# Kernel tuning notes

Hardware: AMD Instinct MI355X
Metric: run time of the kernel (lower is better)

Reference implementation:

```python
import jax, jax.numpy as jnp
import numpy as np

N_NODES = 20000
N_EDGES = 640000
IN_DIM = 128
HID_DIM = 256
N_CLASSES = 3
N_TYPES = 4
N_ASPECTS = 4096


def _type_aware_gcn(x, W_type, W_self, b, src, dst, etypes, n_nodes):
    # Per-node, per-type transforms: [N, T, H]
    xt = jnp.einsum('nd,tdh->nth', x, W_type)
    # Per-edge message: transform of source node under the edge's type. [E, H]
    msg = xt[src, etypes]
    # Degree-normalized scatter-sum into destination nodes.
    agg = jax.ops.segment_sum(msg, dst, num_segments=n_nodes)
    deg = jax.ops.segment_sum(jnp.ones((src.shape[0],), dtype=x.dtype), dst,
                              num_segments=n_nodes)
    agg = agg / jnp.clip(deg, 1.0)[:, None]
    # Self-loop transform + bias.
    return agg + x @ W_self + b


def setup_inputs() -> dict:
    key = jax.random.key(0)
    ks = jax.random.split(key, 12)
    features = jax.random.normal(ks[0], (N_NODES, IN_DIM), dtype=jnp.float32)
    edge_index = jax.random.randint(ks[1], (2, N_EDGES), 0, N_NODES)
    edge_types = jax.random.randint(ks[2], (N_EDGES,), 0, N_TYPES)
    aspect_indices = jax.random.randint(ks[3], (N_ASPECTS,), 0, N_NODES)
    s1 = 1.0 / np.sqrt(IN_DIM)
    s2 = 1.0 / np.sqrt(HID_DIM)
    W_type1 = jax.random.uniform(ks[4], (N_TYPES, IN_DIM, HID_DIM), minval=-s1, maxval=s1)
    W_self1 = jax.random.uniform(ks[5], (IN_DIM, HID_DIM), minval=-s1, maxval=s1)
    b1 = jnp.zeros((HID_DIM,), dtype=jnp.float32)
    W_type2 = jax.random.uniform(ks[6], (N_TYPES, HID_DIM, HID_DIM), minval=-s2, maxval=s2)
    W_self2 = jax.random.uniform(ks[7], (HID_DIM, HID_DIM), minval=-s2, maxval=s2)
    b2 = jnp.zeros((HID_DIM,), dtype=jnp.float32)
    W_cls = jax.random.uniform(ks[8], (HID_DIM, N_CLASSES), minval=-s2, maxval=s2)
    b_cls = jnp.zeros((N_CLASSES,), dtype=jnp.float32)
    return {
        'features': features,
        'W_type1': W_type1, 'W_self1': W_self1, 'b1': b1,
        'W_type2': W_type2, 'W_self2': W_self2, 'b2': b2,
        'W_cls': W_cls, 'b_cls': b_cls,
        'edge_index': edge_index,
        'edge_types': edge_types,
        'aspect_indices': aspect_indices,
    }


def reference(features, W_type1, W_self1, b1, W_type2, W_self2, b2,
              W_cls, b_cls, edge_index, edge_types, aspect_indices):
    n = features.shape[0]
    src, dst = edge_index[0], edge_index[1]
    h = _type_aware_gcn(features, W_type1, W_self1, b1, src, dst, edge_types, n)
    h = jax.nn.relu(h)
    # dropout: eval mode -> identity
    h = _type_aware_gcn(h, W_type2, W_self2, b2, src, dst, edge_types, n)
    aspect_embeddings = h[aspect_indices]            # [A, H]
    logits = aspect_embeddings @ W_cls + b_cls       # [A, C]
    return logits
```

## Files before the change

kernel.cpp:

```cpp
#include <hip/hip_runtime.h>

#define N_NODES   20000
#define N_EDGES   640000
#define IN_DIM    128
#define HID_DIM   256
#define N_TYPES   4
#define N_ASPECTS 4096
#define NT4       (N_NODES * N_TYPES)
#define NBUCK     157
#define BCAP      5120
#define CHUNK     2560

typedef __bf16 v8bf __attribute__((ext_vector_type(8)));
typedef float  f32x4 __attribute__((ext_vector_type(4)));
typedef float  v2f   __attribute__((ext_vector_type(2)));

static __device__ __forceinline__ float bf2f(unsigned short u) {
    return __builtin_bit_cast(float, ((unsigned int)u) << 16);
}
static __device__ __forceinline__ float bflo(unsigned int u) {
    return __builtin_bit_cast(float, u << 16);
}
static __device__ __forceinline__ float bfhi(unsigned int u) {
    return __builtin_bit_cast(float, u & 0xffff0000u);
}
static __device__ __forceinline__ unsigned short f2bf(float f) {
    unsigned int u = __builtin_bit_cast(unsigned int, f);
    u += 0x7fffu + ((u >> 16) & 1u);
    return (unsigned short)(u >> 16);
}

static __device__ __forceinline__ void gload16(const unsigned short* g, unsigned short* l) {
    __builtin_amdgcn_global_load_lds(
        (const __attribute__((address_space(1))) void*)g,
        (__attribute__((address_space(3))) void*)l,
        16, 0, 0);
}

static __device__ __forceinline__ int local_flag(const unsigned short* w, int* red) {
    int tid = threadIdx.x;
    int c = 0;
    for (int i = tid; i < 1024; i += 256) {
        unsigned hb = (w[i] >> 8) & 0x7f;
        c += (hb >= 0x39 && hb <= 0x3D) ? 1 : 0;
    }
#pragma unroll
    for (int off = 32; off >= 1; off >>= 1) c += __shfl_down(c, off);
    if ((tid & 63) == 0) red[tid >> 6] = c;
    __syncthreads();
    int tot = red[0] + red[1] + red[2] + red[3];
    __syncthreads();
    return (tot >= 768) ? 1 : 0;
}

__global__ __launch_bounds__(256) void prepA_kernel(
        const void* __restrict__ x,
        const void* __restrict__ Ws1, const void* __restrict__ Wt1,
        const void* __restrict__ Ws2, const void* __restrict__ Wt2,
        const int* __restrict__ ei, const int* __restrict__ et,
        unsigned short* __restrict__ xc,
        unsigned int* __restrict__ xc8,
        unsigned short* __restrict__ WT1,
        unsigned short* __restrict__ WT2,
        int* __restrict__ bucket_cursor,
        unsigned int* __restrict__ breg,
        int* __restrict__ flag) {
    __shared__ __align__(16) char smem[14336];
    int b = blockIdx.x, tid = threadIdx.x;
    if (b < 250) {
        unsigned int* ord = (unsigned int*)smem;
        int* hist  = (int*)(smem + 10240);
        int* start = hist + NBUCK;
        int* cur   = start + NBUCK;
        int* gbase = cur + NBUCK;
        int* sbuf  = gbase + NBUCK;
        int e0 = b * CHUNK;
        for (int i = tid; i < NBUCK; i += 256) hist[i] = 0;
        __syncthreads();
        unsigned int pk[10];
        int bk[10];
#pragma unroll
        for (int r = 0; r < 10; r++) {
            int e = e0 + r * 256 + tid;
            int s = __builtin_nontemporal_load(ei + e);
            int d = __builtin_nontemporal_load(ei + N_EDGES + e);
            int t = __builtin_nontemporal_load(et + e);
            pk[r] = (unsigned int)s | ((unsigned int)t << 15) | ((unsigned int)d << 17);
            bk[r] = d >> 7;
            atomicAdd(&hist[bk[r]], 1);
        }
        __syncthreads();
        int v = (tid < NBUCK) ? hist[tid] : 0;
        sbuf[tid] = v;
        __syncthreads();
        for (int o = 1; o < 256; o <<= 1) {
            int t = (tid >= o) ? sbuf[tid - o] : 0;
            __syncthreads();
            sbuf[tid] += t;
            __syncthreads();
        }
        if (tid < NBUCK) { start[tid] = sbuf[tid] - v; cur[tid] = sbuf[tid] - v; }
        __syncthreads();
#pragma unroll
        for (int r = 0; r < 10; r++) {
            int p = atomicAdd(&cur[bk[r]], 1);
            ord[p] = pk[r];
        }
        __syncthreads();
        for (int bb = tid; bb < NBUCK; bb += 256)
            if (hist[bb] > 0) gbase[bb] = atomicAdd(bucket_cursor + bb, hist[bb]);
        __syncthreads();
        for (int p = tid; p < CHUNK; p += 256) {
            unsigned int e = ord[p];
            int bb = (int)(e >> 24);
            int gp = gbase[bb] + (p - start[bb]);
            if (gp < BCAP)
                __builtin_nontemporal_store(e, breg + (size_t)bb * BCAP + gp);
        }
    } else if (b < 1500) {
        int bf = local_flag((const unsigned short*)Ws1, (int*)smem);
        int idx = (b - 250) * 256 + tid;
        float f[8];
        if (bf) {
            uint4 v = reinterpret_cast<const uint4*>(x)[idx];
            reinterpret_cast<uint4*>(xc)[idx] = v;
            f[0] = bflo(v.x); f[1] = bfhi(v.x);
            f[2] = bflo(v.y); f[3] = bfhi(v.y);
            f[4] = bflo(v.z); f[5] = bfhi(v.z);
            f[6] = bflo(v.w); f[7] = bfhi(v.w);
        } else {
            const float* xf = reinterpret_cast<const float*>(x) + (size_t)idx * 8;
            unsigned short r[8] __attribute__((aligned(16)));
#pragma unroll
            for (int j = 0; j < 8; j++) { f[j] = xf[j]; r[j] = f2bf(xf[j]); }
            reinterpret_cast<uint4*>(xc)[idx] = *reinterpret_cast<const uint4*>(r);
        }
        int lo = 0, hi = 0;
        lo = __builtin_amdgcn_cvt_pk_fp8_f32(f[0], f[1], lo, false);
        lo = __builtin_amdgcn_cvt_pk_fp8_f32(f[2], f[3], lo, true);
        hi = __builtin_amdgcn_cvt_pk_fp8_f32(f[4], f[5], hi, false);
        hi = __builtin_amdgcn_cvt_pk_fp8_f32(f[6], f[7], hi, true);
        xc8[idx * 2]     = (unsigned int)lo;
        xc8[idx * 2 + 1] = (unsigned int)hi;
    } else if (b < 2140) {
        int bf = local_flag((const unsigned short*)Ws1, (int*)smem);
        int idx = (b - 1500) * 256 + tid;
        int n = idx / 640, k = idx - n * 640;
        const void* p = (k < 128) ? Ws1 : Wt1;
        size_t src = (k < 128) ? ((size_t)k * 256 + n) : ((size_t)(k - 128) * 256 + n);
        WT1[idx] = bf ? ((const unsigned short*)p)[src] : f2bf(((const float*)p)[src]);
    } else if (b < 3420) {
        int bf = local_flag((const unsigned short*)Ws1, (int*)smem);
        int idx = (b - 2140) * 256 + tid;
        int n = idx / 1280, k = idx - n * 1280;
        const void* p = (k < 256) ? Ws2 : Wt2;
        size_t src = (k < 256) ? ((size_t)k * 256 + n) : ((size_t)(k - 256) * 256 + n);
        WT2[idx] = bf ? ((const unsigned short*)p)[src] : f2bf(((const float*)p)[src]);
    } else {
        int bf = local_flag((const unsigned short*)Ws1, (int*)smem);
        if (tid == 0) *flag = bf;
    }
}

__global__ __launch_bounds__(256) void bucketB_kernel(
        const unsigned int* __restrict__ breg,
        const int* __restrict__ bucket_cursor,
        unsigned short* __restrict__ perm,
        int* __restrict__ offsets4) {
    __shared__ int cnt[512], off[512];
    __shared__ int buf[256], pscan[256];
    int b = blockIdx.x, tid = threadIdx.x;
    int cv = (tid < NBUCK) ? bucket_cursor[tid] : 0;
    if (cv > BCAP) cv = BCAP;
    buf[tid] = cv;
    __syncthreads();
    for (int o = 1; o < 256; o <<= 1) {
        int t = (tid >= o) ? buf[tid - o] : 0;
        __syncthreads();
        buf[tid] += t;
        __syncthreads();
    }
    int obase = (b > 0) ? buf[b - 1] : 0;
    if (b == 0 && tid == 0) offsets4[NT4] = buf[255];
    int Eb = bucket_cursor[b];
    if (Eb > BCAP) Eb = BCAP;
    for (int i = tid; i < 512; i += 256) cnt[i] = 0;
    __syncthreads();
    const unsigned int* reg = breg + (size_t)b * BCAP;
    for (int i = tid; i < Eb; i += 256) {
        unsigned int e = reg[i];
        int seg = (((e >> 17) & 127) << 2) | ((e >> 15) & 3);
        atomicAdd(&cnt[seg], 1);
    }
    __syncthreads();
    int pv = cnt[2 * tid] + cnt[2 * tid + 1];
    pscan[tid] = pv;
    __syncthreads();
    for (int o = 1; o < 256; o <<= 1) {
        int t = (tid >= o) ? pscan[tid - o] : 0;
        __syncthreads();
        pscan[tid] += t;
        __syncthreads();
    }
    int pexcl = pscan[tid] - pv;
    off[2 * tid]     = pexcl;
    off[2 * tid + 1] = pexcl + cnt[2 * tid];
    __syncthreads();
    for (int i = tid; i < 512; i += 256) {
        int node = b * 128 + (i >> 2);
        if (node < N_NODES) offsets4[node * 4 + (i & 3)] = obase + off[i];
    }
    __syncthreads();
    for (int i = tid; i < Eb; i += 256) {
        unsigned int e = reg[i];
        int seg = (((e >> 17) & 127) << 2) | ((e >> 15) & 3);
        int p = atomicAdd(&off[seg], 1);
        perm[obase + p] = (unsigned short)(e & 0x7fff);
    }
}

template <int D>
__global__ __launch_bounds__(256) void agg8_kernel(
        const unsigned int* __restrict__ F8,
        const int* __restrict__ offs4,
        const unsigned short* __restrict__ perm,
        unsigned short* __restrict__ AG) {
    constexpr int G = D / 8;
    constexpr int NSUB = 64 / G;
    int wave = threadIdx.x >> 6, lane = threadIdx.x & 63;
    int sg = lane / G;
    int gl = lane - sg * G;
    for (int n = blockIdx.x * 4 + wave; n < N_NODES; n += gridDim.x * 4) {
        int o0 = offs4[n * 4];
        int o4 = offs4[n * 4 + 4];
        int deg = o4 - o0;
        float inv = 1.0f / (float)(deg > 1 ? deg : 1);
        int s0 = o0;
#pragma unroll
        for (int t = 0; t < 4; t++) {
            int s1 = offs4[n * 4 + t + 1];
            float a[8];
#pragma unroll
            for (int v = 0; v < 8; v++) a[v] = 0.f;
            int j = s0;
            while (j < s1) {
                int m = s1 - j;
                if (m > 64) m = 64;
                int pw = (int)perm[j + ((lane < m) ? lane : 0)];
                int nfull = (m / (NSUB * 4)) * (NSUB * 4);
                for (int base = 0; base < nfull; base += NSUB * 4) {
                    uint2 x[4];
#pragma unroll
                    for (int l = 0; l < 4; l++) {
                        int src = __shfl(pw, base + sg * 4 + l);
                        x[l] = *reinterpret_cast<const uint2*>(F8 + (size_t)src * (D / 4) + gl * 2);
                    }
#pragma unroll
                    for (int l = 0; l < 4; l++) {
                        v2f p0 = __builtin_amdgcn_cvt_pk_f32_fp8((int)x[l].x, false);
                        v2f p1 = __builtin_amdgcn_cvt_pk_f32_fp8((int)x[l].x, true);
                        v2f p2 = __builtin_amdgcn_cvt_pk_f32_fp8((int)x[l].y, false);
                        v2f p3 = __builtin_amdgcn_cvt_pk_f32_fp8((int)x[l].y, true);
                        a[0] += p0.x; a[1] += p0.y;
                        a[2] += p1.x; a[3] += p1.y;
                        a[4] += p2.x; a[5] += p2.y;
                        a[6] += p3.x; a[7] += p3.y;
                    }
                }
                for (int k = nfull; k < m; k += NSUB) {
                    int e = k + sg;
                    int valid = (e < m);
                    int idx = valid ? e : (m - 1);
                    int src = __shfl(pw, idx);
                    uint2 x = *reinterpret_cast<const uint2*>(F8 + (size_t)src * (D / 4) + gl * 2);
                    unsigned msk = valid ? 0xffffffffu : 0u;
                    x.x &= msk; x.y &= msk;
                    v2f p0 = __builtin_amdgcn_cvt_pk_f32_fp8((int)x.x, false);
                    v2f p1 = __builtin_amdgcn_cvt_pk_f32_fp8((int)x.x, true);
                    v2f p2 = __builtin_amdgcn_cvt_pk_f32_fp8((int)x.y, false);
                    v2f p3 = __builtin_amdgcn_cvt_pk_f32_fp8((int)x.y, true);
                    a[0] += p0.x; a[1] += p0.y;
                    a[2] += p1.x; a[3] += p1.y;
                    a[4] += p2.x; a[5] += p2.y;
                    a[6] += p3.x; a[7] += p3.y;
                }
                j += m;
            }
#pragma unroll
            for (int v = 0; v < 8; v++) {
                float s = a[v];
                s += __shfl_xor(s, G);
                if (NSUB == 4) s += __shfl_xor(s, 2 * G);
                a[v] = s * inv;
            }
            if (sg == 0) {
                unsigned short r[8] __attribute__((aligned(16)));
#pragma unroll
                for (int v = 0; v < 8; v++) r[v] = f2bf(a[v]);
                *reinterpret_cast<uint4*>(AG + (size_t)n * (4 * D) + t * D + gl * 8) =
                    *reinterpret_cast<const uint4*>(r);
            }
            s0 = s1;
        }
    }
}

template <int D>
__global__ __launch_bounds__(256) void gemm_kernel(
        const unsigned short* __restrict__ X,
        const unsigned short* __restrict__ AG,
        const unsigned short* __restrict__ BT,
        const void* __restrict__ bias,
        const int* __restrict__ flagp,
        unsigned short* __restrict__ C,
        unsigned char* __restrict__ C8,
        int M, int relu) {
    constexpr int K = 5 * D;
    __shared__ __align__(16) unsigned short As[128 * 64];
    __shared__ __align__(16) unsigned short Bs[128 * 64];
    int b = blockIdx.x;
    int mt = (b >> 4) * 8 + (b & 7);
    int nt = (b >> 3) & 1;
    int mtiles = (M + 127) >> 7;
    if (mt >= mtiles) return;
    int m0 = mt * 128;
    int n0 = nt * 128;
    int tid  = threadIdx.x;
    int wave = tid >> 6, lane = tid & 63;
    int wm = wave >> 1, wn = wave & 1;
    int quad = lane >> 4, l16 = lane & 15;

    f32x4 acc[4][4];
#pragma unroll
    for (int i = 0; i < 4; i++)
#pragma unroll
        for (int j = 0; j < 4; j++) acc[i][j] = (f32x4){0.f, 0.f, 0.f, 0.f};

    for (int k0 = 0; k0 < K; k0 += 64) {
        const unsigned short* abase = (k0 < D) ? X : AG;
        int rs  = (k0 < D) ? D : 4 * D;
        int col = (k0 < D) ? k0 : (k0 - D);
#pragma unroll
        for (int p = 0; p < 4; p++) {
            int c   = p * 256 + tid;
            int row = c >> 3;
            int c8  = c & 7;
            int gr  = m0 + row;
            if (gr >= M) gr = M - 1;
            gload16(abase + (size_t)gr * rs + col + c8 * 8, &As[c * 8]);
        }
#pragma unroll
        for (int p = 0; p < 4; p++) {
            int c   = p * 256 + tid;
            int row = c >> 3;
            int c8  = c & 7;
            gload16(BT + (size_t)(n0 + row) * K + k0 + c8 * 8, &Bs[c * 8]);
        }
        __syncthreads();
#pragma unroll
        for (int ks = 0; ks < 2; ks++) {
            v8bf af[4], bfr[4];
#pragma unroll
            for (int i = 0; i < 4; i++)
                af[i] = *reinterpret_cast<const v8bf*>(
                    &As[(wm * 64 + i * 16 + l16) * 64 + ks * 32 + quad * 8]);
#pragma unroll
            for (int j = 0; j < 4; j++)
                bfr[j] = *reinterpret_cast<const v8bf*>(
                    &Bs[(wn * 64 + j * 16 + l16) * 64 + ks * 32 + quad * 8]);
#pragma unroll
            for (int i = 0; i < 4; i++)
#pragma unroll
                for (int j = 0; j < 4; j++)
                    acc[i][j] = __builtin_amdgcn_mfma_f32_16x16x32_bf16(af[i], bfr[j], acc[i][j], 0, 0, 0);
        }
        __syncthreads();
    }
    int bf = *flagp;
#pragma unroll
    for (int i = 0; i < 4; i++) {
#pragma unroll
        for (int j = 0; j < 4; j++) {
            int col = n0 + wn * 64 + j * 16 + l16;
            float bv = bf ? bf2f(((const unsigned short*)bias)[col])
                          : ((const float*)bias)[col];
#pragma unroll
            for (int r = 0; r < 4; r++) {
                int row = m0 + wm * 64 + i * 16 + quad * 4 + r;
                if (row < M) {
                    float v = acc[i][j][r] + bv;
                    if (relu) v = fmaxf(v, 0.0f);
                    C[(size_t)row * 256 + col] = f2bf(v);
                    if (C8) {
                        int pk = __builtin_amdgcn_cvt_pk_fp8_f32(v, v, 0, false);
                        C8[(size_t)row * 256 + col] = (unsigned char)(pk & 0xff);
                    }
                }
            }
        }
    }
}

__global__ void cls_kernel(const unsigned short* __restrict__ h2,
                           const int* __restrict__ aidx,
                           const void* __restrict__ Wc,
                           const void* __restrict__ bc,
                           const int* __restrict__ flagp,
                           void* __restrict__ out) {
    int lin = blockIdx.x * blockDim.x + threadIdx.x;
    int a = lin >> 6, lane = lin & 63;
    if (a >= N_ASPECTS) return;
    int bf = *flagp;
    int node = aidx[a];
    uint2 v = *reinterpret_cast<const uint2*>(h2 + (size_t)node * 256 + lane * 4);
    float hv[4] = {bflo(v.x), bfhi(v.x), bflo(v.y), bfhi(v.y)};
    float a0 = 0.f, a1 = 0.f, a2 = 0.f;
#pragma unroll
    for (int r = 0; r < 4; r++) {
        int k = lane * 4 + r;
        float w0 = bf ? bf2f(((const unsigned short*)Wc)[k * 3 + 0]) : ((const float*)Wc)[k * 3 + 0];
        float w1 = bf ? bf2f(((const unsigned short*)Wc)[k * 3 + 1]) : ((const float*)Wc)[k * 3 + 1];
        float w2 = bf ? bf2f(((const unsigned short*)Wc)[k * 3 + 2]) : ((const float*)Wc)[k * 3 + 2];
        a0 += hv[r] * w0;
        a1 += hv[r] * w1;
        a2 += hv[r] * w2;
    }
#pragma unroll
    for (int off = 32; off >= 1; off >>= 1) {
        a0 += __shfl_down(a0, off);
        a1 += __shfl_down(a1, off);
        a2 += __shfl_down(a2, off);
    }
    if (lane == 0) {
        float b0 = bf ? bf2f(((const unsigned short*)bc)[0]) : ((const float*)bc)[0];
        float b1 = bf ? bf2f(((const unsigned short*)bc)[1]) : ((const float*)bc)[1];
        float b2 = bf ? bf2f(((const unsigned short*)bc)[2]) : ((const float*)bc)[2];
        if (bf) {
            unsigned short* o = (unsigned short*)out;
            o[a * 3 + 0] = f2bf(a0 + b0);
            o[a * 3 + 1] = f2bf(a1 + b1);
            o[a * 3 + 2] = f2bf(a2 + b2);
        } else {
            float* o = (float*)out;
            o[a * 3 + 0] = a0 + b0;
            o[a * 3 + 1] = a1 + b1;
            o[a * 3 + 2] = a2 + b2;
        }
    }
}

extern "C" void kernel_launch(void* const* d_in, const int* in_sizes, int n_in,
                              void* d_out, int out_size, void* d_ws, size_t ws_size,
                              hipStream_t stream) {
    const void* x   = d_in[0];
    const void* Wt1 = d_in[1];
    const void* Ws1 = d_in[2];
    const void* b1  = d_in[3];
    const void* Wt2 = d_in[4];
    const void* Ws2 = d_in[5];
    const void* b2  = d_in[6];
    const void* Wc  = d_in[7];
    const void* bc  = d_in[8];
    const int* ei = (const int*)d_in[9];
    const int* et = (const int*)d_in[10];
    const int* ai = (const int*)d_in[11];

    char* ws = (char*)d_ws;
    size_t off = 0;
    auto alloc = [&](size_t bytes) {
        void* p = ws + off;
        off += (bytes + 255) & ~(size_t)255;
        return p;
    };
    int*            flag          = (int*)alloc(4);
    int*            bucket_cursor = (int*)alloc((size_t)NBUCK * 4);
    int*            offsets4      = (int*)alloc((size_t)(NT4 + 1) * 4);
    unsigned int*   breg          = (unsigned int*)alloc((size_t)NBUCK * BCAP * 4);
    unsigned short* perm          = (unsigned short*)alloc((size_t)N_EDGES * 2);
    unsigned short* xc            = (unsigned short*)alloc((size_t)N_NODES * IN_DIM * 2);
    unsigned int*   xc8           = (unsigned int*)alloc((size_t)N_NODES * IN_DIM);
    unsigned short* AG            = (unsigned short*)alloc((size_t)N_NODES * 4 * HID_DIM * 2);
    unsigned short* h             = (unsigned short*)alloc((size_t)N_NODES * HID_DIM * 2);
    unsigned char*  h8            = (unsigned char*)alloc((size_t)N_NODES * HID_DIM);
    unsigned short* h2            = (unsigned short*)alloc((size_t)N_NODES * HID_DIM * 2);
    unsigned short* WT1           = (unsigned short*)alloc((size_t)640 * 256 * 2);
    unsigned short* WT2           = (unsigned short*)alloc((size_t)1280 * 256 * 2);

    hipMemsetAsync(bucket_cursor, 0, (size_t)NBUCK * 4, stream);
    prepA_kernel<<<3421, 256, 0, stream>>>(x, Ws1, Wt1, Ws2, Wt2, ei, et,
                                           xc, xc8, WT1, WT2, bucket_cursor, breg, flag);
    bucketB_kernel<<<NBUCK, 256, 0, stream>>>(breg, bucket_cursor, perm, offsets4);

    agg8_kernel<IN_DIM><<<4096, 256, 0, stream>>>(xc8, offsets4, perm, AG);
    gemm_kernel<IN_DIM><<<320, 256, 0, stream>>>(xc, AG, WT1, b1, flag, h, h8, N_NODES, 1);
    agg8_kernel<HID_DIM><<<4096, 256, 0, stream>>>((const unsigned int*)h8, offsets4, perm, AG);
    gemm_kernel<HID_DIM><<<320, 256, 0, stream>>>(h, AG, WT2, b2, flag, h2, nullptr, N_NODES, 0);
    cls_kernel<<<(N_ASPECTS * 64) / 256, 256, 0, stream>>>(h2, ai, Wc, bc, flag, d_out);
}
```

Measured before the change: 244.4 us.

## Double-buffer LDS tiles in GEMM kernel to overlap loads with MFMA

Adds a second LDS buffer for the A and B tiles in the fused GEMM and prefetches the next K-step's tiles while the current step's MFMAs run, removing one barrier per iteration. The aim is to hide global-to-LDS load latency behind compute. In exchange, LDS use per block doubles to 64KB, which may cut occupancy. Correctness depends on gload16 being synchronous or properly waited on before the barrier.

After: 241.3 us. Within noise of the previous version (-1.3%).

```diff
diff --git a/kernel.cpp b/kernel.cpp
--- a/kernel.cpp
+++ b/kernel.cpp
@@ -316,8 +316,9 @@
         unsigned char* __restrict__ C8,
         int M, int relu) {
     constexpr int K = 5 * D;
-    __shared__ __align__(16) unsigned short As[128 * 64];
-    __shared__ __align__(16) unsigned short Bs[128 * 64];
+    constexpr int NSTEP = K / 64;
+    __shared__ __align__(16) unsigned short As[2 * 128 * 64];
+    __shared__ __align__(16) unsigned short Bs[2 * 128 * 64];
     int b = blockIdx.x;
     int mt = (b >> 4) * 8 + (b & 7);
     int nt = (b >> 3) & 1;
@@ -336,38 +337,50 @@
 #pragma unroll
         for (int j = 0; j < 4; j++) acc[i][j] = (f32x4){0.f, 0.f, 0.f, 0.f};
 
-    for (int k0 = 0; k0 < K; k0 += 64) {
+    int srow = tid >> 3;
+    int sc8  = tid & 7;
+
+    auto stage = [&](int t, int buf) {
+        int k0 = t * 64;
         const unsigned short* abase = (k0 < D) ? X : AG;
         int rs  = (k0 < D) ? D : 4 * D;
         int col = (k0 < D) ? k0 : (k0 - D);
+        unsigned short* As_ = As + buf * (128 * 64);
+        unsigned short* Bs_ = Bs + buf * (128 * 64);
 #pragma unroll
         for (int p = 0; p < 4; p++) {
             int c   = p * 256 + tid;
-            int row = c >> 3;
-            int c8  = c & 7;
+            int row = srow + p * 32;
             int gr  = m0 + row;
             if (gr >= M) gr = M - 1;
-            gload16(abase + (size_t)gr * rs + col + c8 * 8, &As[c * 8]);
+            gload16(abase + (size_t)gr * rs + col + sc8 * 8, As_ + c * 8);
         }
 #pragma unroll
         for (int p = 0; p < 4; p++) {
             int c   = p * 256 + tid;
-            int row = c >> 3;
-            int c8  = c & 7;
-            gload16(BT + (size_t)(n0 + row) * K + k0 + c8 * 8, &Bs[c * 8]);
-        }
-        __syncthreads();
+            int row = srow + p * 32;
+            gload16(BT + (size_t)(n0 + row) * K + k0 + sc8 * 8, Bs_ + c * 8);
+        }
+    };
+
+    stage(0, 0);
+    __syncthreads();
+    int cur = 0;
+    for (int t = 0; t < NSTEP; t++) {
+        if (t + 1 < NSTEP) stage(t + 1, cur ^ 1);
+        const unsigned short* As_ = As + cur * (128 * 64);
+        const unsigned short* Bs_ = Bs + cur * (128 * 64);
 #pragma unroll
         for (int ks = 0; ks < 2; ks++) {
             v8bf af[4], bfr[4];
 #pragma unroll
             for (int i = 0; i < 4; i++)
                 af[i] = *reinterpret_cast<const v8bf*>(
-                    &As[(wm * 64 + i * 16 + l16) * 64 + ks * 32 + quad * 8]);
+                    &As_[(wm * 64 + i * 16 + l16) * 64 + ks * 32 + quad * 8]);
 #pragma unroll
             for (int j = 0; j < 4; j++)
                 bfr[j] = *reinterpret_cast<const v8bf*>(
-                    &Bs[(wn * 64 + j * 16 + l16) * 64 + ks * 32 + quad * 8]);
+                    &Bs_[(wn * 64 + j * 16 + l16) * 64 + ks * 32 + quad * 8]);
 #pragma unroll
             for (int i = 0; i < 4; i++)
 #pragma unroll
@@ -375,6 +388,7 @@
                     acc[i][j] = __builtin_amdgcn_mfma_f32_16x16x32_bf16(af[i], bfr[j], acc[i][j], 0, 0, 0);
         }
         __syncthreads();
+        cur ^= 1;
     }
     int bf = *flagp;
 #pragma unroll
```

## Restructure GEMM: register-direct A fragments, double-buffered padded B tiles, narrower N tiles

Applied to the files above, without the earlier changes.

The GEMM kernel now loads A fragments straight from global memory into registers, skipping the LDS staging. B is prefetched two steps ahead into registers and written into a double-buffered, padded (stride 72) LDS tile, which lets loads overlap the MFMA compute. The N tile is cut from 128 to 64 columns and the grid doubled to 640 blocks to add parallelism. In exchange, A reads are no longer shared through LDS, so the same A rows are fetched by four N tiles. Global traffic for A also rises, and correctness depends on hand-placed waitcnt and barrier ordering.

Measured after the change: 310.6 us. +27.1%, slower.

```diff
diff --git a/kernel.cpp b/kernel.cpp
--- a/kernel.cpp
+++ b/kernel.cpp
@@ -30,12 +30,10 @@
     return (unsigned short)(u >> 16);
 }
 
-static __device__ __forceinline__ void gload16(const unsigned short* g, unsigned short* l) {
-    __builtin_amdgcn_global_load_lds(
-        (const __attribute__((address_space(1))) void*)g,
-        (__attribute__((address_space(3))) void*)l,
-        16, 0, 0);
-}
+#define LGKM0() do { asm volatile("s_waitcnt lgkmcnt(0)" ::: "memory"); \
+                     __builtin_amdgcn_sched_barrier(0); } while (0)
+#define BAR()   do { __builtin_amdgcn_s_barrier(); \
+                     __builtin_amdgcn_sched_barrier(0); } while (0)
 
 static __device__ __forceinline__ int local_flag(const unsigned short* w, int* red) {
     int tid = threadIdx.x;
@@ -316,72 +314,110 @@
         unsigned char* __restrict__ C8,
         int M, int relu) {
     constexpr int K = 5 * D;
-    __shared__ __align__(16) unsigned short As[128 * 64];
-    __shared__ __align__(16) unsigned short Bs[128 * 64];
+    constexpr int NSTEP = K / 64;
+    __shared__ __align__(16) unsigned short Bs[2 * 64 * 72];
     int b = blockIdx.x;
-    int mt = (b >> 4) * 8 + (b & 7);
-    int nt = (b >> 3) & 1;
+    int nt = (b >> 3) & 3;
+    int mt = (b >> 5) * 8 + (b & 7);
     int mtiles = (M + 127) >> 7;
     if (mt >= mtiles) return;
     int m0 = mt * 128;
-    int n0 = nt * 128;
+    int n0 = nt * 64;
     int tid  = threadIdx.x;
     int wave = tid >> 6, lane = tid & 63;
     int wm = wave >> 1, wn = wave & 1;
     int quad = lane >> 4, l16 = lane & 15;
 
-    f32x4 acc[4][4];
+    f32x4 acc[4][2];
 #pragma unroll
     for (int i = 0; i < 4; i++)
 #pragma unroll
-        for (int j = 0; j < 4; j++) acc[i][j] = (f32x4){0.f, 0.f, 0.f, 0.f};
-
-    for (int k0 = 0; k0 < K; k0 += 64) {
+        for (int j = 0; j < 2; j++) acc[i][j] = (f32x4){0.f, 0.f, 0.f, 0.f};
+
+    int brow = tid >> 3;
+    int bc8  = tid & 7;
+
+    auto loadB = [&](int t, uint4 (&br)[2]) {
+        int k0 = t * 64;
+        const unsigned short* bp = BT + (size_t)(n0 + brow) * K + k0 + bc8 * 8;
+        br[0] = *reinterpret_cast<const uint4*>(bp);
+        br[1] = *reinterpret_cast<const uint4*>(bp + (size_t)32 * K);
+    };
+    auto writeB = [&](const uint4 (&br)[2], int buf) {
+        unsigned short* base = Bs + buf * (64 * 72);
+        *reinterpret_cast<uint4*>(base + brow * 72 + bc8 * 8) = br[0];
+        *reinterpret_cast<uint4*>(base + (32 + brow) * 72 + bc8 * 8) = br[1];
+    };
+    auto loadA = [&](int t, v8bf (&afc)[4][2]) {
+        int k0 = t * 64;
         const unsigned short* abase = (k0 < D) ? X : AG;
         int rs  = (k0 < D) ? D : 4 * D;
         int col = (k0 < D) ? k0 : (k0 - D);
 #pragma unroll
-        for (int p = 0; p < 4; p++) {
-            int c   = p * 256 + tid;
-            int row = c >> 3;
-            int c8  = c & 7;
-            int gr  = m0 + row;
+        for (int i = 0; i < 4; i++) {
+            int gr = m0 + wm * 64 + i * 16 + l16;
             if (gr >= M) gr = M - 1;
-            gload16(abase + (size_t)gr * rs + col + c8 * 8, &As[c * 8]);
-        }
-#pragma unroll
-        for (int p = 0; p < 4; p++) {
-            int c   = p * 256 + tid;
-            int row = c >> 3;
-            int c8  = c & 7;
-            gload16(BT + (size_t)(n0 + row) * K + k0 + c8 * 8, &Bs[c * 8]);
-        }
-        __syncthreads();
+            const unsigned short* rp = abase + (size_t)gr * rs + col + quad * 8;
+            afc[i][0] = *reinterpret_cast<const v8bf*>(rp);
+            afc[i][1] = *reinterpret_cast<const v8bf*>(rp + 32);
+        }
+    };
+    auto compute = [&](int cur, const v8bf (&afc)[4][2]) {
+        const unsigned short* base = Bs + cur * (64 * 72);
 #pragma unroll
         for (int ks = 0; ks < 2; ks++) {
-            v8bf af[4], bfr[4];
+            v8bf bfr[2];
+#pragma unroll
+            for (int j = 0; j < 2; j++)
+                bfr[j] = *reinterpret_cast<const v8bf*>(
+                    base + (wn * 32 + j * 16 + l16) * 72 + ks * 32 + quad * 8);
 #pragma unroll
             for (int i = 0; i < 4; i++)
-                af[i] = *reinterpret_cast<const v8bf*>(
-                    &As[(wm * 64 + i * 16 + l16) * 64 + ks * 32 + quad * 8]);
-#pragma unroll
-            for (int j = 0; j < 4; j++)
-                bfr[j] = *reinterpret_cast<const v8bf*>(
-                    &Bs[(wn * 64 + j * 16 + l16) * 64 + ks * 32 + quad * 8]);
-#pragma unroll
-            for (int i = 0; i < 4; i++)
-#pragma unroll
-                for (int j = 0; j < 4; j++)
-                    acc[i][j] = __builtin_amdgcn_mfma_f32_16x16x32_bf16(af[i], bfr[j], acc[i][j], 0, 0, 0);
-        }
-        __syncthreads();
-    }
+#pragma unroll
+                for (int j = 0; j < 2; j++)
+                    acc[i][j] = __builtin_amdgcn_mfma_f32_16x16x32_bf16(
+                        afc[i][ks], bfr[j], acc[i][j], 0, 0, 0);
+        }
+    };
+
+    v8bf afA[4][2], afB[4][2];
+    uint4 brA[2], brB[2];
+
+    {
+        uint4 t0[2];
+        loadB(0, t0);
+        loadA(0, afA);
+        loadB(1, brA);
+        writeB(t0, 0);
+        LGKM0();
+        BAR();
+    }
+
+    auto step = [&](int t, int cur,
+                    const v8bf (&afc)[4][2], v8bf (&afn)[4][2],
+                    uint4 (&brc)[2], uint4 (&brn)[2]) {
+        if (t + 2 < NSTEP) loadB(t + 2, brn);
+        if (t + 1 < NSTEP) loadA(t + 1, afn);
+        compute(cur, afc);
+        BAR();
+        if (t + 1 < NSTEP) {
+            writeB(brc, cur ^ 1);
+            LGKM0();
+        }
+        BAR();
+    };
+
+    for (int t = 0; t < NSTEP; t += 2) {
+        step(t,     0, afA, afB, brA, brB);
+        step(t + 1, 1, afB, afA, brB, brA);
+    }
+
     int bf = *flagp;
 #pragma unroll
     for (int i = 0; i < 4; i++) {
 #pragma unroll
-        for (int j = 0; j < 4; j++) {
-            int col = n0 + wn * 64 + j * 16 + l16;
+        for (int j = 0; j < 2; j++) {
+            int col = n0 + wn * 32 + j * 16 + l16;
             float bv = bf ? bf2f(((const unsigned short*)bias)[col])
                           : ((const float*)bias)[col];
 #pragma unroll
@@ -492,8 +528,8 @@
     bucketB_kernel<<<NBUCK, 256, 0, stream>>>(breg, bucket_cursor, perm, offsets4);
 
     agg8_kernel<IN_DIM><<<4096, 256, 0, stream>>>(xc8, offsets4, perm, AG);
-    gemm_kernel<IN_DIM><<<320, 256, 0, stream>>>(xc, AG, WT1, b1, flag, h, h8, N_NODES, 1);
+    gemm_kernel<IN_DIM><<<640, 256, 0, stream>>>(xc, AG, WT1, b1, flag, h, h8, N_NODES, 1);
     agg8_kernel<HID_DIM><<<4096, 256, 0, stream>>>((const unsigned int*)h8, offsets4, perm, AG);
-    gemm_kernel<HID_DIM><<<320, 256, 0, stream>>>(h, AG, WT2, b2, flag, h2, nullptr, N_NODES, 0);
+    gemm_kernel<HID_DIM><<<640, 256, 0, stream>>>(h, AG, WT2, b2, flag, h2, nullptr, N_NODES, 0);
     cls_kernel<<<(N_ASPECTS * 64) / 256, 256, 0, stream>>>(h2, ai, Wc, bc, flag, d_out);
 }
```
